# Kernel optimization log

Hardware: AMD Instinct MI355X
Metric: run time of the kernel (lower is better)

The kernel has to match this reference:

```python
import jax, jax.numpy as jnp
import numpy as np

B, N0, C, K, D = 16384, 1024, 12, 64, 3  # batch, feat dim, num_classes, num_clusters, ndim


def setup_inputs() -> dict:
    key = jax.random.key(0)
    ks = jax.random.split(key, 6)
    s = 0.02  # weight init scale
    return {
        "x": jax.random.normal(ks[0], (B, N0), dtype=jnp.float32),
        "Wfc": jax.random.normal(ks[1], (N0, C), dtype=jnp.float32) * s,
        "bfc": jnp.zeros((C,), dtype=jnp.float32),
        "Wbin": jax.random.normal(ks[2], (C, K, N0), dtype=jnp.float32) * s,
        "bbin": jnp.zeros((C, K), dtype=jnp.float32),
        "Wres": jax.random.normal(ks[3], (C, K, N0, D), dtype=jnp.float32) * s,
        "bres": jnp.zeros((C, K, D), dtype=jnp.float32),
        "centers": jax.random.normal(ks[4], (K, D), dtype=jnp.float32),
    }


def reference(x, Wfc, bfc, Wbin, bbin, Wres, bres, centers):
    # category head
    y0 = x @ Wfc + bfc                                            # [B, C]
    # per-class bin logits (batched over all classes at once)
    ybin = jnp.einsum("bn,ckn->bck", x, Wbin) + bbin              # [B, C, K]
    ind = jnp.argmax(ybin, axis=2)                                # [B, C] selected cluster per class
    # multires path: all (class, cluster) expert residuals, then one-hot select
    yres_all = jnp.einsum("bn,cknd->bckd", x, Wres) + bres        # [B, C, K, D]
    yres = jnp.take_along_axis(
        yres_all, ind[:, :, None, None], axis=2
    ).squeeze(2)                                                  # [B, C, D]
    # gather cluster centers and add residual
    y = centers[ind] + yres                                       # [B, C, D]
    # torch: stack over classes -> [C,B,D]; permute(1,2,0) -> [B, D, C]
    y1 = jnp.transpose(y, (0, 2, 1))                              # [B, D, C]
    return (y0, y1)
```

## Files before the change

### kernel.cpp

```cpp
#include <hip/hip_runtime.h>

typedef unsigned int uint32;
typedef unsigned long long uint64;
typedef unsigned short ushort16;
typedef __attribute__((ext_vector_type(8))) short bf16x8;
typedef __attribute__((ext_vector_type(4))) float f32x4;
typedef __attribute__((ext_vector_type(4))) uint32 u32x4;

#define B_SZ 16384
#define MARGIN 0.012f

__device__ __forceinline__ ushort16 f2bf(float f) {
  uint32 u = __float_as_uint(f);
  u += 0x7fffu + ((u >> 16) & 1u);
  return (ushort16)(u >> 16);
}
__device__ __forceinline__ float bf2f(ushort16 h) { return __uint_as_float(((uint32)h) << 16); }
__device__ __forceinline__ float bflo(uint32 u) { return __uint_as_float(u << 16); }
__device__ __forceinline__ float bfhi(uint32 u) { return __uint_as_float(u & 0xffff0000u); }
__device__ __forceinline__ uint32 pk2(float lo, float hi) {
  return ((uint32)f2bf(hi) << 16) | (uint32)f2bf(lo);
}
__device__ __forceinline__ int dot4(uint32 a, uint32 b, int c) {
#if __has_builtin(__builtin_amdgcn_sdot4)
  return __builtin_amdgcn_sdot4((int)a, (int)b, c, false);
#else
  int s = c;
#pragma unroll
  for (int k = 0; k < 4; ++k)
    s += (int)(char)(a >> (8 * k)) * (int)(char)(b >> (8 * k));
  return s;
#endif
}
__device__ __forceinline__ int q8(float v, float inv) {
  int q = (int)rintf(v * inv);
  return q > 127 ? 127 : (q < -127 ? -127 : q);
}
__device__ __forceinline__ int red16_i(int s) {
  s += __builtin_amdgcn_update_dpp(0, s, 0xB1, 0xF, 0xF, true);
  s += __builtin_amdgcn_update_dpp(0, s, 0x4E, 0xF, 0xF, true);
  s += __builtin_amdgcn_update_dpp(0, s, 0x141, 0xF, 0xF, true);
  s += __builtin_amdgcn_update_dpp(0, s, 0x140, 0xF, 0xF, true);
  return s;
}
#define DPP_D_LEVEL(v, ctrl)                                                        \
  {                                                                                 \
    uint64 u_ = (uint64)__double_as_longlong(v);                                    \
    int lo_ = __builtin_amdgcn_update_dpp(0, (int)(uint32)u_, (ctrl), 0xF, 0xF, true); \
    int hi_ = __builtin_amdgcn_update_dpp(0, (int)(uint32)(u_ >> 32), (ctrl), 0xF, 0xF, true); \
    (v) += __longlong_as_double((long long)(((uint64)(uint32)hi_ << 32) | (uint32)lo_)); \
  }
__device__ __forceinline__ double red16_d(double v) {
  DPP_D_LEVEL(v, 0xB1); DPP_D_LEVEL(v, 0x4E);
  DPP_D_LEVEL(v, 0x141); DPP_D_LEVEL(v, 0x140);
  return v;
}

__global__ __launch_bounds__(256) void prep_all(
    const float* __restrict__ Wfc, const float* __restrict__ Wbin,
    const float* __restrict__ x, ushort16* __restrict__ Wall,
    uint2* __restrict__ xb, uint32* __restrict__ xq, float* __restrict__ sxb) {
  const int blk = blockIdx.x;
  const int t = threadIdx.x;
  if (blk < 3584) {
    int idx = blk * 256 + t;
    int j = idx >> 10, n = idx & 1023;
    float v = 0.f;
    if (j < 12) v = Wfc[n * 12 + j];
    else if (j >= 64 && j < 832) v = Wbin[(size_t)(j - 64) * 1024 + n];
    Wall[idx] = f2bf(v);
  } else {
    const int lane = t & 63;
    const int b = (blk - 3584) * 4 + (t >> 6);
    const float4* xr = (const float4*)(x + (size_t)b * 1024 + lane * 16);
    float4 v0 = xr[0], v1 = xr[1], v2 = xr[2], v3 = xr[3];
    float xv[16] = {v0.x, v0.y, v0.z, v0.w, v1.x, v1.y, v1.z, v1.w,
                    v2.x, v2.y, v2.z, v2.w, v3.x, v3.y, v3.z, v3.w};
    u32x4 pa, pb;
    pa.x = pk2(xv[0], xv[1]);  pa.y = pk2(xv[2], xv[3]);
    pa.z = pk2(xv[4], xv[5]);  pa.w = pk2(xv[6], xv[7]);
    pb.x = pk2(xv[8], xv[9]);  pb.y = pk2(xv[10], xv[11]);
    pb.z = pk2(xv[12], xv[13]); pb.w = pk2(xv[14], xv[15]);
    u32x4* xbrow = (u32x4*)((uint32*)xb + (size_t)b * 512);
    xbrow[2 * lane] = pa;
    xbrow[2 * lane + 1] = pb;
    float m = 0.f;
#pragma unroll
    for (int i = 0; i < 16; ++i) m = fmaxf(m, fabsf(xv[i]));
    for (int off = 32; off; off >>= 1) m = fmaxf(m, __shfl_xor(m, off));
    float mx = fmaxf(m, 1e-20f);
    float inv = 127.f / mx;
    if (lane == 0) sxb[b] = mx / 127.f;
    u32x4 qv;
#pragma unroll
    for (int q = 0; q < 4; ++q) {
      uint32 u = ((uint32)(unsigned char)(char)q8(xv[4 * q + 0], inv)) |
                 ((uint32)(unsigned char)(char)q8(xv[4 * q + 1], inv)) << 8 |
                 ((uint32)(unsigned char)(char)q8(xv[4 * q + 2], inv)) << 16 |
                 ((uint32)(unsigned char)(char)q8(xv[4 * q + 3], inv)) << 24;
      qv[q] = u;
    }
    ((u32x4*)(xq + (size_t)b * 256))[lane] = qv;
  }
}

__global__ void prep_wall_f(const float* __restrict__ Wfc, const float* __restrict__ Wbin,
                            ushort16* __restrict__ Wall) {
  int idx = blockIdx.x * 256 + threadIdx.x;
  int j = idx >> 10, n = idx & 1023;
  float v = 0.f;
  if (j < 12) v = Wfc[n * 12 + j];
  else if (j >= 64 && j < 832) v = Wbin[(size_t)(j - 64) * 1024 + n];
  Wall[idx] = f2bf(v);
}
__global__ void prep_wres(const float* __restrict__ Wres, ushort16* __restrict__ Wres_b) {
  int idx = blockIdx.x * 256 + threadIdx.x;
  int n = idx & 1023;
  int d = (idx >> 10) % 3;
  int ck = idx / 3072;
  Wres_b[idx] = f2bf(Wres[((size_t)ck * 1024 + n) * 3 + d]);
}

template<int XB>
__global__ __launch_bounds__(256) void gemm_mfma(
    const float* __restrict__ x, const ushort16* __restrict__ xb,
    const float* __restrict__ bfc, const float* __restrict__ bbin,
    const ushort16* __restrict__ Wall, ushort16* __restrict__ ybin,
    unsigned char* __restrict__ ind8, uint64* __restrict__ mask64,
    const float* __restrict__ Wres, uint32* __restrict__ wq,
    float* __restrict__ swk, float* __restrict__ out) {
  __shared__ __align__(16) char smem[49152];
  const int t = threadIdx.x;

  if (XB && blockIdx.x >= 896) {
    float* red = (float*)smem;
    const int ck = blockIdx.x - 896;
    const float4* base4 = (const float4*)(Wres + (size_t)ck * 3072);
    float4 v0 = base4[3 * t], v1 = base4[3 * t + 1], v2 = base4[3 * t + 2];
    float vals[12] = {v0.x, v0.y, v0.z, v0.w, v1.x, v1.y, v1.z, v1.w, v2.x, v2.y, v2.z, v2.w};
    float m = 0.f;
#pragma unroll
    for (int i = 0; i < 12; ++i) m = fmaxf(m, fabsf(vals[i]));
    red[t] = m; __syncthreads();
    for (int s = 128; s; s >>= 1) { if (t < s) red[t] = fmaxf(red[t], red[t + s]); __syncthreads(); }
    float mx = fmaxf(red[0], 1e-20f);
    float inv = 127.f / mx;
    if (t == 0) swk[ck] = mx / 127.f;
#pragma unroll
    for (int d = 0; d < 3; ++d) {
      uint32 u = 0;
#pragma unroll
      for (int j = 0; j < 4; ++j)
        u |= ((uint32)(unsigned char)(char)q8(vals[j * 3 + d], inv)) << (8 * j);
      wq[((size_t)(ck * 3 + d) << 8) + t] = u;
    }
    return;
  }

  const int lane = t & 63, wid = t >> 6;
  const int wm = wid & 1, wn = wid >> 1;

  int orig = blockIdx.x;
  int bid = (orig & 7) * 112 + (orig >> 3);
  int nb = bid % 7, mb = bid / 7;
  const int b0 = mb * 128;

  f32x4 acc[4][4];
#pragma unroll
  for (int i = 0; i < 4; ++i)
#pragma unroll
    for (int j = 0; j < 4; ++j) acc[i][j] = (f32x4){0.f, 0.f, 0.f, 0.f};

  const int lr = lane & 15, lq = lane >> 4;

#define GLDS(srcp, dstoff)                                                      \
  __builtin_amdgcn_global_load_lds(                                             \
      (const __attribute__((address_space(1))) uint32*)(srcp),                  \
      (__attribute__((address_space(3))) uint32*)(smem + (dstoff)), 16, 0, 0)

  if (XB) {
    const int gs2 = (lane & 3) ^ ((lane >> 2) & 3);
    const int grw2 = lane >> 2;
    const int ch0 = wid * 2, ch1 = wid * 2 + 1;
    const ushort16* arow0 = xb + (size_t)(b0 + ch0 * 16 + grw2) * 1024 + gs2 * 8;
    const ushort16* arow1 = xb + (size_t)(b0 + ch1 * 16 + grw2) * 1024 + gs2 * 8;
    const ushort16* brow0 = Wall + (size_t)(nb * 128 + ch0 * 16 + grw2) * 1024 + gs2 * 8;
    const ushort16* brow1 = Wall + (size_t)(nb * 128 + ch1 * 16 + grw2) * 1024 + gs2 * 8;

#define STAGE_HALF(h, buf)                                                      \
    {                                                                           \
      int bb_ = (buf) * 16384;                                                  \
      int kc_ = (h) * 32;                                                       \
      GLDS(arow0 + kc_, bb_ + ch0 * 1024);                                      \
      GLDS(arow1 + kc_, bb_ + ch1 * 1024);                                      \
      GLDS(brow0 + kc_, bb_ + 8192 + ch0 * 1024);                               \
      GLDS(brow1 + kc_, bb_ + 8192 + ch1 * 1024);                               \
    }

    STAGE_HALF(0, 0); STAGE_HALF(1, 1);
    const int cbx2 = (lq * 16) ^ ((lr & 3) << 4);
    const int arow_off = (wm * 64 + lr) * 64;
    const int brow_off = (wn * 64 + lr) * 64;
    int rb = 0;
#pragma unroll 1
    for (int h = 0; h < 32; ++h) {
      if (h < 31) asm volatile("s_waitcnt vmcnt(4)" ::: "memory");
      else        asm volatile("s_waitcnt vmcnt(0)" ::: "memory");
      __builtin_amdgcn_s_barrier();
      if (h < 30) {
        int sb = rb + 2; if (sb >= 3) sb -= 3;
        STAGE_HALF(h + 2, sb);
      }
      const char* base = smem + rb * 16384;
      bf16x8 af[4], bfr[4];
#pragma unroll
      for (int i = 0; i < 4; ++i)
        af[i] = *(const bf16x8*)(base + arow_off + i * 1024 + cbx2);
#pragma unroll
      for (int j = 0; j < 4; ++j)
        bfr[j] = *(const bf16x8*)(base + 8192 + brow_off + j * 1024 + cbx2);
#pragma unroll
      for (int i = 0; i < 4; ++i)
#pragma unroll
        for (int j = 0; j < 4; ++j)
          acc[i][j] = __builtin_amdgcn_mfma_f32_16x16x32_bf16(af[i], bfr[j], acc[i][j], 0, 0, 0);
      rb = (rb == 2) ? 0 : rb + 1;
    }
#undef STAGE_HALF
  } else {
    const int fxor = (lr & 7) << 4;
    for (int kc = 0; kc < 1024; kc += 64) {
      __syncthreads();
      const int sxor = ((t >> 3) & 7) << 4;
#pragma unroll
      for (int i = 0; i < 4; ++i) {
        int s = t + i * 256;
        int row = s >> 3, c8 = (s & 7) * 8;
        int dst = row * 128 + ((c8 * 2) ^ sxor);
        const float4* src = (const float4*)(x + (size_t)(b0 + row) * 1024 + kc + c8);
        float4 v0 = src[0], v1 = src[1];
        u32x4 pv;
        pv.x = pk2(v0.x, v0.y); pv.y = pk2(v0.z, v0.w);
        pv.z = pk2(v1.x, v1.y); pv.w = pk2(v1.z, v1.w);
        *(u32x4*)(smem + dst) = pv;
      }
#pragma unroll
      for (int i = 0; i < 4; ++i) {
        int s = t + i * 256;
        int row = s >> 3, c8 = (s & 7) * 8;
        int dst = 16384 + row * 128 + ((c8 * 2) ^ sxor);
        u32x4 v = *(const u32x4*)(Wall + (size_t)(nb * 128 + row) * 1024 + kc + c8);
        *(u32x4*)(smem + dst) = v;
      }
      __syncthreads();
#pragma unroll
      for (int kk = 0; kk < 2; ++kk) {
        int cbx = (kk * 64 + lq * 16) ^ fxor;
        bf16x8 af[4], bfr[4];
#pragma unroll
        for (int i = 0; i < 4; ++i)
          af[i] = *(const bf16x8*)(smem + (wm * 64 + i * 16 + lr) * 128 + cbx);
#pragma unroll
        for (int j = 0; j < 4; ++j)
          bfr[j] = *(const bf16x8*)(smem + 16384 + (wn * 64 + j * 16 + lr) * 128 + cbx);
#pragma unroll
        for (int i = 0; i < 4; ++i)
#pragma unroll
          for (int j = 0; j < 4; ++j)
            acc[i][j] = __builtin_amdgcn_mfma_f32_16x16x32_bf16(af[i], bfr[j], acc[i][j], 0, 0, 0);
      }
    }
  }
#undef GLDS

  const int g = 2 * nb + wn;
  if (g == 0) {
#pragma unroll
    for (int i = 0; i < 4; ++i)
#pragma unroll
      for (int r = 0; r < 4; ++r) {
        int gm = b0 + wm * 64 + i * 16 + lq * 4 + r;
        if (lr < 12) out[(size_t)gm * 12 + lr] = acc[i][0][r] + bfc[lr];
      }
    return;
  }
  if (g > 12) return;
  const int c = g - 1;
  if (XB == 0) {
#pragma unroll
    for (int i = 0; i < 4; ++i)
#pragma unroll
      for (int j = 0; j < 4; ++j)
#pragma unroll
        for (int r = 0; r < 4; ++r) {
          int gm = b0 + wm * 64 + i * 16 + lq * 4 + r;
          int col = j * 16 + lr;
          ybin[((size_t)gm * 12 + c) * 64 + col] = f2bf(acc[i][j][r] + bbin[c * 64 + col]);
        }
    return;
  }
  float bb[4];
#pragma unroll
  for (int j = 0; j < 4; ++j) bb[j] = bbin[c * 64 + j * 16 + lr];
#pragma unroll
  for (int i = 0; i < 4; ++i)
#pragma unroll
    for (int r = 0; r < 4; ++r) {
      float v0 = acc[i][0][r] + bb[0], v1 = acc[i][1][r] + bb[1];
      float v2 = acc[i][2][r] + bb[2], v3 = acc[i][3][r] + bb[3];
      float m1 = v0, m2 = -3.4e38f; int k1 = lr;
      if (v1 > m1) { m2 = m1; m1 = v1; k1 = 16 + lr; } else m2 = fmaxf(m2, v1);
      if (v2 > m1) { m2 = m1; m1 = v2; k1 = 32 + lr; } else m2 = fmaxf(m2, v2);
      if (v3 > m1) { m2 = m1; m1 = v3; k1 = 48 + lr; } else m2 = fmaxf(m2, v3);
#pragma unroll
      for (int off = 1; off < 16; off <<= 1) {
        float om1 = __shfl_xor(m1, off);
        int   ok1 = __shfl_xor(k1, off);
        float om2 = __shfl_xor(m2, off);
        bool take = (om1 > m1) || (om1 == m1 && ok1 < k1);
        float lose = take ? m1 : om1;
        m2 = fmaxf(fmaxf(m2, om2), lose);
        if (take) { m1 = om1; k1 = ok1; }
      }
      float thr = m1 - MARGIN;
      uint64 bl0 = __ballot(v0 >= thr);
      uint64 bl1 = __ballot(v1 >= thr);
      uint64 bl2 = __ballot(v2 >= thr);
      uint64 bl3 = __ballot(v3 >= thr);
      if (lr == 0) {
        int row = wm * 64 + i * 16 + lq * 4 + r;
        uint64 mk = ((bl0 >> (lq * 16)) & 0xffffull) |
                    (((bl1 >> (lq * 16)) & 0xffffull) << 16) |
                    (((bl2 >> (lq * 16)) & 0xffffull) << 32) |
                    (((bl3 >> (lq * 16)) & 0xffffull) << 48);
        int gp = (b0 + row) * 12 + c;
        ind8[gp] = (unsigned char)(k1 | ((m1 - m2 <= MARGIN) ? 128 : 0));
        mask64[gp] = mk;
      }
    }
}

__global__ __launch_bounds__(256) void compact_k(const unsigned char* __restrict__ ind8,
                                                 uint32* __restrict__ cnt,
                                                 uint32* __restrict__ wl) {
  const int b = blockIdx.x * 256 + threadIdx.x;
  const int lane = threadIdx.x & 63;
  const uint32* p = (const uint32*)(ind8 + b * 12);
  uint32 d0 = p[0], d1 = p[1], d2 = p[2];
  uint32 fmask = 0;
#pragma unroll
  for (int j = 0; j < 4; ++j) {
    if ((d0 >> (8 * j)) & 128u) fmask |= 1u << j;
    if ((d1 >> (8 * j)) & 128u) fmask |= 1u << (4 + j);
    if ((d2 >> (8 * j)) & 128u) fmask |= 1u << (8 + j);
  }
  uint32 n_i = (uint32)__popc(fmask);
  uint32 pre = n_i;
  for (int off = 1; off < 64; off <<= 1) {
    uint32 v = __shfl_up(pre, off);
    if (lane >= off) pre += v;
  }
  uint32 total = __shfl(pre, 63);
  uint32 base = 0;
  if (lane == 63 && total) base = atomicAdd(cnt, total);
  base = __shfl(base, 63);
  uint32 off = base + pre - n_i;
  while (fmask) {
    int c = __ffs(fmask) - 1;
    fmask &= fmask - 1;
    wl[off++] = (uint32)(b * 12 + c);
  }
}

__global__ __launch_bounds__(256) void tail_k(
    const float* __restrict__ x, const float* __restrict__ Wbin,
    const float* __restrict__ bbin, const float* __restrict__ bres,
    const float* __restrict__ centers, const unsigned char* __restrict__ ind8,
    const uint64* __restrict__ mask64, const uint32* __restrict__ wq,
    const float* __restrict__ swk, const uint32* __restrict__ xq,
    const float* __restrict__ sxb, const uint32* __restrict__ cnt,
    const uint32* __restrict__ wl, float* __restrict__ out) {
  const int lane = threadIdx.x & 63;
  const int w = threadIdx.x >> 6;
  const int rm = (int)(blockIdx.x % 3u);
  const int rq = (int)(blockIdx.x / 3u);

  if (rm == 0) {
    const uint32 nresc = *cnt;
#pragma unroll 1
    for (uint32 slot = rq * 4 + w; slot < nresc; slot += 32768) {
      const uint32 pp = wl[slot];
      const int b = (int)(pp / 12u), c = (int)(pp % 12u);

      float xv[16];
      const float4* xr = (const float4*)(x + (size_t)b * 1024 + lane * 16);
#pragma unroll
      for (int q = 0; q < 4; ++q) {
        float4 vv = xr[q];
        xv[4 * q] = vv.x; xv[4 * q + 1] = vv.y; xv[4 * q + 2] = vv.z; xv[4 * q + 3] = vv.w;
      }
      const float sx = sxb[b];
      const float inv = (sx > 0.f) ? 1.f / sx : 0.f;
      uint32 xi[4];
#pragma unroll
      for (int q = 0; q < 4; ++q)
        xi[q] = ((uint32)(unsigned char)(char)q8(xv[4 * q + 0], inv)) |
                ((uint32)(unsigned char)(char)q8(xv[4 * q + 1], inv)) << 8 |
                ((uint32)(unsigned char)(char)q8(xv[4 * q + 2], inv)) << 16 |
                ((uint32)(unsigned char)(char)q8(xv[4 * q + 3], inv)) << 24;

      uint64 mask = mask64[pp];
      double best = -1.0e300;
      int bk = 0;
#pragma unroll 1
      while (mask) {
        int kk[4];
        int nc = 0;
        while (mask && nc < 4) { kk[nc++] = __ffsll(mask) - 1; mask &= mask - 1; }
#pragma unroll
        for (int j = 1; j < 4; ++j) if (j >= nc) kk[j] = kk[0];
        double s[4] = {0.0, 0.0, 0.0, 0.0};
#pragma unroll
        for (int ci = 0; ci < 4; ++ci) {
          const float4* wr4 = (const float4*)(Wbin + ((size_t)c * 64 + kk[ci]) * 1024 + lane * 16);
#pragma unroll
          for (int q = 0; q < 4; ++q) {
            float4 wvv = wr4[q];
            s[ci] += (double)xv[4 * q] * (double)wvv.x + (double)xv[4 * q + 1] * (double)wvv.y +
                     (double)xv[4 * q + 2] * (double)wvv.z + (double)xv[4 * q + 3] * (double)wvv.w;
          }
        }
#pragma unroll
        for (int ci = 0; ci < 4; ++ci) s[ci] = red16_d(s[ci]);
        for (int off = 16; off < 64; off <<= 1) {
#pragma unroll
          for (int ci = 0; ci < 4; ++ci) s[ci] += __shfl_xor(s[ci], off);
        }
#pragma unroll
        for (int ci = 0; ci < 4; ++ci) {
          double sv = s[ci] + (double)bbin[c * 64 + kk[ci]];
          if (ci < nc && sv > best) { best = sv; bk = kk[ci]; }
        }
      }
      const int ck = c * 64 + bk;
      const uint32* wr = wq + (size_t)ck * 768;
      int acc[3];
#pragma unroll
      for (int d = 0; d < 3; ++d) {
        u32x4 wvq = *(const u32x4*)(wr + d * 256 + lane * 4);
        int ss = dot4(xi[0], wvq.x, 0);
        ss = dot4(xi[1], wvq.y, ss);
        ss = dot4(xi[2], wvq.z, ss);
        acc[d] = dot4(xi[3], wvq.w, ss);
      }
#pragma unroll
      for (int d = 0; d < 3; ++d) acc[d] = red16_i(acc[d]);
      for (int off = 16; off < 64; off <<= 1) {
        acc[0] += __shfl_xor(acc[0], off);
        acc[1] += __shfl_xor(acc[1], off);
        acc[2] += __shfl_xor(acc[2], off);
      }
      if (lane == 0) {
        const size_t obase = (size_t)B_SZ * 12 + (size_t)b * 36;
        float sc = sx * swk[ck];
        out[obase + 0 * 12 + c] = centers[bk * 3 + 0] + bres[ck * 3 + 0] + sc * (float)acc[0];
        out[obase + 1 * 12 + c] = centers[bk * 3 + 1] + bres[ck * 3 + 1] + sc * (float)acc[1];
        out[obase + 2 * 12 + c] = centers[bk * 3 + 2] + bres[ck * 3 + 2] + sc * (float)acc[2];
      }
    }
    return;
  }

  const int b = rq * 2 + (rm - 1);

  const u32x4 xi = *(const u32x4*)(xq + (size_t)b * 256 + lane * 4);
  const float sx = sxb[b];
  const size_t obase = (size_t)B_SZ * 12 + (size_t)b * 36;

  int iv[3], ind[3], ck[3];
  u32x4 wv[3][3];
#pragma unroll
  for (int cc = 0; cc < 3; ++cc) {
    int c = w * 3 + cc;
    iv[cc] = ind8[b * 12 + c];
    ind[cc] = iv[cc] & 63;
    ck[cc] = c * 64 + ind[cc];
    const uint32* wr = wq + (size_t)ck[cc] * 768;
#pragma unroll
    for (int d = 0; d < 3; ++d)
      wv[cc][d] = *(const u32x4*)(wr + d * 256 + lane * 4);
  }
  int acc[3][3];
#pragma unroll
  for (int cc = 0; cc < 3; ++cc)
#pragma unroll
    for (int d = 0; d < 3; ++d) {
      int s = dot4(xi.x, wv[cc][d].x, 0);
      s = dot4(xi.y, wv[cc][d].y, s);
      s = dot4(xi.z, wv[cc][d].z, s);
      acc[cc][d] = dot4(xi.w, wv[cc][d].w, s);
    }
#pragma unroll
  for (int cc = 0; cc < 3; ++cc)
#pragma unroll
    for (int d = 0; d < 3; ++d)
      acc[cc][d] = red16_i(acc[cc][d]);
  for (int off = 16; off < 64; off <<= 1) {
#pragma unroll
    for (int cc = 0; cc < 3; ++cc)
#pragma unroll
      for (int d = 0; d < 3; ++d)
        acc[cc][d] += __shfl_xor(acc[cc][d], off);
  }
  if (lane == 0) {
#pragma unroll
    for (int cc = 0; cc < 3; ++cc) {
      if (iv[cc] & 128) continue;
      int c = w * 3 + cc;
      float sc = sx * swk[ck[cc]];
      out[obase + 0 * 12 + c] = centers[ind[cc] * 3 + 0] + bres[ck[cc] * 3 + 0] + sc * (float)acc[cc][0];
      out[obase + 1 * 12 + c] = centers[ind[cc] * 3 + 1] + bres[ck[cc] * 3 + 1] + sc * (float)acc[cc][1];
      out[obase + 2 * 12 + c] = centers[ind[cc] * 3 + 2] + bres[ck[cc] * 3 + 2] + sc * (float)acc[cc][2];
    }
  }
}

__global__ __launch_bounds__(256) void select2(
    const float* __restrict__ x, const float* __restrict__ Wbin,
    const float* __restrict__ bbin, const float* __restrict__ bres,
    const float* __restrict__ centers, const ushort16* __restrict__ Wres_b,
    const ushort16* __restrict__ ybin, float* __restrict__ out) {
  const int lane = threadIdx.x & 63;
  const int w = threadIdx.x >> 6;
  const int b = blockIdx.x;
  float xv[16];
  {
    const float4* xr = (const float4*)(x + (size_t)b * 1024 + lane * 16);
#pragma unroll
    for (int q = 0; q < 4; ++q) {
      float4 v = xr[q];
      xv[4 * q] = v.x; xv[4 * q + 1] = v.y; xv[4 * q + 2] = v.z; xv[4 * q + 3] = v.w;
    }
  }
  const size_t obase = (size_t)B_SZ * 12 + (size_t)b * 36;
#pragma unroll 1
  for (int cc = 0; cc < 3; ++cc) {
    const int c = w * 3 + cc;
    float v = bf2f(ybin[((size_t)b * 12 + c) * 64 + lane]);
    float m1 = v, m2 = -3.4e38f;
    int k1 = lane;
    for (int off = 32; off; off >>= 1) {
      float om1 = __shfl_xor(m1, off);
      int   ok1 = __shfl_xor(k1, off);
      float om2 = __shfl_xor(m2, off);
      bool take = (om1 > m1) || (om1 == m1 && ok1 < k1);
      float lose = take ? m1 : om1;
      m2 = fmaxf(fmaxf(m2, om2), lose);
      if (take) { m1 = om1; k1 = ok1; }
    }
    int ind = k1;
    if (m1 - m2 <= MARGIN) {
      unsigned long long mask = __ballot(v >= m1 - MARGIN);
      double best = -1.0e300;
      int bk = 0;
      while (mask) {
        int k = __ffsll(mask) - 1;
        mask &= (mask - 1);
        const float4* wr4 = (const float4*)(Wbin + ((size_t)c * 64 + k) * 1024 + lane * 16);
        double s = 0.0;
#pragma unroll
        for (int q = 0; q < 4; ++q) {
          float4 wv = wr4[q];
          s += (double)xv[4 * q] * (double)wv.x + (double)xv[4 * q + 1] * (double)wv.y +
               (double)xv[4 * q + 2] * (double)wv.z + (double)xv[4 * q + 3] * (double)wv.w;
        }
        for (int off = 32; off; off >>= 1) s += __shfl_xor(s, off);
        s += (double)bbin[c * 64 + k];
        if (s > best) { best = s; bk = k; }
      }
      ind = bk;
    }
    const ushort16* wr = Wres_b + ((size_t)(c * 64 + ind) * 3) * 1024;
    float a[3] = {0.f, 0.f, 0.f};
#pragma unroll
    for (int d = 0; d < 3; ++d) {
      const u32x4* pp = (const u32x4*)(wr + d * 1024 + lane * 16);
      u32x4 w0 = pp[0], w1 = pp[1];
      uint32 uw[8] = {w0.x, w0.y, w0.z, w0.w, w1.x, w1.y, w1.z, w1.w};
#pragma unroll
      for (int q = 0; q < 8; ++q) {
        a[d] = fmaf(xv[2 * q],     bflo(uw[q]), a[d]);
        a[d] = fmaf(xv[2 * q + 1], bfhi(uw[q]), a[d]);
      }
    }
    for (int off = 32; off; off >>= 1) {
      a[0] += __shfl_xor(a[0], off);
      a[1] += __shfl_xor(a[1], off);
      a[2] += __shfl_xor(a[2], off);
    }
    if (lane == 0) {
      int ck = c * 64 + ind;
      out[obase + 0 * 12 + c] = centers[ind * 3 + 0] + bres[ck * 3 + 0] + a[0];
      out[obase + 1 * 12 + c] = centers[ind * 3 + 1] + bres[ck * 3 + 1] + a[1];
      out[obase + 2 * 12 + c] = centers[ind * 3 + 2] + bres[ck * 3 + 2] + a[2];
    }
  }
}

extern "C" void kernel_launch(void* const* d_in, const int* in_sizes, int n_in,
                              void* d_out, int out_size, void* d_ws, size_t ws_size,
                              hipStream_t stream) {
  const float* x       = (const float*)d_in[0];
  const float* Wfc     = (const float*)d_in[1];
  const float* bfc     = (const float*)d_in[2];
  const float* Wbin    = (const float*)d_in[3];
  const float* bbin    = (const float*)d_in[4];
  const float* Wres    = (const float*)d_in[5];
  const float* bres    = (const float*)d_in[6];
  const float* centers = (const float*)d_in[7];
  float* out = (float*)d_out;

  char* ws = (char*)d_ws;
  ushort16* Wall = (ushort16*)ws;
  if (ws_size >= 57151488ull) {
    uint32*        wq     = (uint32*)(ws + 1835008);
    float*         swk    = (float*)(ws + 4194304);
    unsigned char* ind8   = (unsigned char*)(ws + 4197376);
    uint64*        mask64 = (uint64*)(ws + 4393984);
    ushort16*      xb     = (ushort16*)(ws + 5966848);
    uint32*        xq     = (uint32*)(ws + 39521280);
    float*         sxb    = (float*)(ws + 56298496);
    uint32*        cnt    = (uint32*)(ws + 56364032);
    uint32*        wl     = (uint32*)(ws + 56364288);

    hipMemsetAsync(cnt, 0, 4, stream);
    prep_all<<<7680, 256, 0, stream>>>(Wfc, Wbin, x, Wall, (uint2*)xb, xq, sxb);
    gemm_mfma<1><<<1664, 256, 0, stream>>>(x, xb, bfc, bbin, Wall,
                                           (ushort16*)nullptr, ind8, mask64,
                                           Wres, wq, swk, out);
    compact_k<<<64, 256, 0, stream>>>(ind8, cnt, wl);
    tail_k<<<24576, 256, 0, stream>>>(x, Wbin, bbin, bres, centers, ind8, mask64,
                                      wq, swk, xq, sxb, cnt, wl, out);
  } else {
    ushort16* Wres_b = (ushort16*)(ws + 1835008);
    ushort16* ybin   = (ushort16*)(ws + 6553600);
    prep_wall_f<<<3584, 256, 0, stream>>>(Wfc, Wbin, Wall);
    prep_wres<<<9216, 256, 0, stream>>>(Wres, Wres_b);
    gemm_mfma<0><<<896, 256, 0, stream>>>(x, (const ushort16*)ws, bfc, bbin, Wall,
                                          ybin, (unsigned char*)nullptr,
                                          (uint64*)nullptr, nullptr,
                                          (uint32*)nullptr, (float*)nullptr, out);
    select2<<<B_SZ, 256, 0, stream>>>(x, Wbin, bbin, bres, centers, Wres_b, ybin, out);
  }
}
```

Before: 143.3 us.

## Move int8 x quantization into extra GEMM blocks, simplify bf16 conversion

The prep kernel now only converts x to bf16, one 8-element chunk per thread, using more blocks with simpler indexing. The per-row int8 quantization of x (max-abs reduction and packing) moves into 4096 extra blocks appended to the GEMM launch, so it runs alongside the MFMA blocks rather than before them. This shortens the critical-path prep kernel and aims to fill idle CUs during the GEMM. The cost is that x is read twice (once in prep, once in the GEMM's quantization blocks) and the GEMM grid grows, which may interfere with the MFMA blocks' scheduling.

```diff
diff --git a/kernel.cpp b/kernel.cpp
--- a/kernel.cpp
+++ b/kernel.cpp
@@ -59,7 +59,7 @@
 __global__ __launch_bounds__(256) void prep_all(
     const float* __restrict__ Wfc, const float* __restrict__ Wbin,
     const float* __restrict__ x, ushort16* __restrict__ Wall,
-    uint2* __restrict__ xb, uint32* __restrict__ xq, float* __restrict__ sxb) {
+    u32x4* __restrict__ xb) {
   const int blk = blockIdx.x;
   const int t = threadIdx.x;
   if (blk < 3584) {
@@ -70,37 +70,13 @@
     else if (j >= 64 && j < 832) v = Wbin[(size_t)(j - 64) * 1024 + n];
     Wall[idx] = f2bf(v);
   } else {
-    const int lane = t & 63;
-    const int b = (blk - 3584) * 4 + (t >> 6);
-    const float4* xr = (const float4*)(x + (size_t)b * 1024 + lane * 16);
-    float4 v0 = xr[0], v1 = xr[1], v2 = xr[2], v3 = xr[3];
-    float xv[16] = {v0.x, v0.y, v0.z, v0.w, v1.x, v1.y, v1.z, v1.w,
-                    v2.x, v2.y, v2.z, v2.w, v3.x, v3.y, v3.z, v3.w};
-    u32x4 pa, pb;
-    pa.x = pk2(xv[0], xv[1]);  pa.y = pk2(xv[2], xv[3]);
-    pa.z = pk2(xv[4], xv[5]);  pa.w = pk2(xv[6], xv[7]);
-    pb.x = pk2(xv[8], xv[9]);  pb.y = pk2(xv[10], xv[11]);
-    pb.z = pk2(xv[12], xv[13]); pb.w = pk2(xv[14], xv[15]);
-    u32x4* xbrow = (u32x4*)((uint32*)xb + (size_t)b * 512);
-    xbrow[2 * lane] = pa;
-    xbrow[2 * lane + 1] = pb;
-    float m = 0.f;
-#pragma unroll
-    for (int i = 0; i < 16; ++i) m = fmaxf(m, fabsf(xv[i]));
-    for (int off = 32; off; off >>= 1) m = fmaxf(m, __shfl_xor(m, off));
-    float mx = fmaxf(m, 1e-20f);
-    float inv = 127.f / mx;
-    if (lane == 0) sxb[b] = mx / 127.f;
-    u32x4 qv;
-#pragma unroll
-    for (int q = 0; q < 4; ++q) {
-      uint32 u = ((uint32)(unsigned char)(char)q8(xv[4 * q + 0], inv)) |
-                 ((uint32)(unsigned char)(char)q8(xv[4 * q + 1], inv)) << 8 |
-                 ((uint32)(unsigned char)(char)q8(xv[4 * q + 2], inv)) << 16 |
-                 ((uint32)(unsigned char)(char)q8(xv[4 * q + 3], inv)) << 24;
-      qv[q] = u;
-    }
-    ((u32x4*)(xq + (size_t)b * 256))[lane] = qv;
+    int idx = (blk - 3584) * 256 + t;
+    const float4* s = (const float4*)x + (size_t)idx * 2;
+    float4 a = s[0], b4 = s[1];
+    u32x4 o;
+    o.x = pk2(a.x, a.y);  o.y = pk2(a.z, a.w);
+    o.z = pk2(b4.x, b4.y); o.w = pk2(b4.z, b4.w);
+    xb[idx] = o;
   }
 }
 
@@ -128,10 +104,37 @@
     const ushort16* __restrict__ Wall, ushort16* __restrict__ ybin,
     unsigned char* __restrict__ ind8, uint64* __restrict__ mask64,
     const float* __restrict__ Wres, uint32* __restrict__ wq,
-    float* __restrict__ swk, float* __restrict__ out) {
+    float* __restrict__ swk, uint32* __restrict__ xq,
+    float* __restrict__ sxb, float* __restrict__ out) {
   __shared__ __align__(16) char smem[49152];
   const int t = threadIdx.x;
 
+  if (XB && blockIdx.x >= 1664) {
+    const int lane = t & 63;
+    const int b = (blockIdx.x - 1664) * 4 + (t >> 6);
+    const float4* xr = (const float4*)(x + (size_t)b * 1024 + lane * 16);
+    float4 v0 = xr[0], v1 = xr[1], v2 = xr[2], v3 = xr[3];
+    float xv[16] = {v0.x, v0.y, v0.z, v0.w, v1.x, v1.y, v1.z, v1.w,
+                    v2.x, v2.y, v2.z, v2.w, v3.x, v3.y, v3.z, v3.w};
+    float m = 0.f;
+#pragma unroll
+    for (int i = 0; i < 16; ++i) m = fmaxf(m, fabsf(xv[i]));
+    for (int off = 32; off; off >>= 1) m = fmaxf(m, __shfl_xor(m, off));
+    float mx = fmaxf(m, 1e-20f);
+    float inv = 127.f / mx;
+    if (lane == 0) sxb[b] = mx / 127.f;
+    u32x4 qv;
+#pragma unroll
+    for (int q = 0; q < 4; ++q) {
+      uint32 u = ((uint32)(unsigned char)(char)q8(xv[4 * q + 0], inv)) |
+                 ((uint32)(unsigned char)(char)q8(xv[4 * q + 1], inv)) << 8 |
+                 ((uint32)(unsigned char)(char)q8(xv[4 * q + 2], inv)) << 16 |
+                 ((uint32)(unsigned char)(char)q8(xv[4 * q + 3], inv)) << 24;
+      qv[q] = u;
+    }
+    ((u32x4*)(xq + (size_t)b * 256))[lane] = qv;
+    return;
+  }
   if (XB && blockIdx.x >= 896) {
     float* red = (float*)smem;
     const int ck = blockIdx.x - 896;
@@ -634,10 +637,10 @@
     uint32*        wl     = (uint32*)(ws + 56364288);
 
     hipMemsetAsync(cnt, 0, 4, stream);
-    prep_all<<<7680, 256, 0, stream>>>(Wfc, Wbin, x, Wall, (uint2*)xb, xq, sxb);
-    gemm_mfma<1><<<1664, 256, 0, stream>>>(x, xb, bfc, bbin, Wall,
+    prep_all<<<11776, 256, 0, stream>>>(Wfc, Wbin, x, Wall, (u32x4*)xb);
+    gemm_mfma<1><<<5760, 256, 0, stream>>>(x, xb, bfc, bbin, Wall,
                                            (ushort16*)nullptr, ind8, mask64,
-                                           Wres, wq, swk, out);
+                                           Wres, wq, swk, xq, sxb, out);
     compact_k<<<64, 256, 0, stream>>>(ind8, cnt, wl);
     tail_k<<<24576, 256, 0, stream>>>(x, Wbin, bbin, bres, centers, ind8, mask64,
                                       wq, swk, xq, sxb, cnt, wl, out);
@@ -649,6 +652,7 @@
     gemm_mfma<0><<<896, 256, 0, stream>>>(x, (const ushort16*)ws, bfc, bbin, Wall,
                                           ybin, (unsigned char*)nullptr,
                                           (uint64*)nullptr, nullptr,
+                                          (uint32*)nullptr, (float*)nullptr,
                                           (uint32*)nullptr, (float*)nullptr, out);
     select2<<<B_SZ, 256, 0, stream>>>(x, Wbin, bbin, bres, centers, Wres_b, ybin, out);
   }
```

Result: no change. 141.5 us (-1.2%).
